# Performance work log

Measured on AMD Instinct MI355X. Metric: run time of the kernel, lower is better.

The kernel has to match this reference:

```python
import jax, jax.numpy as jnp
import numpy as np

T, B, N, D, H = 128, 64, 24, 256, 8
F = D // H  # 32


def setup_inputs() -> dict:
    key = jax.random.key(0)
    ks = jax.random.split(key, 7)
    s = 1.0 / np.sqrt(D)  # torch nn.Linear default init range
    inputs = jax.random.normal(ks[0], (T, B, N * D), dtype=jnp.float32)
    Wk = jax.random.uniform(ks[1], (H, F, D), minval=-s, maxval=s, dtype=jnp.float32)
    bk = jax.random.uniform(ks[2], (H, F), minval=-s, maxval=s, dtype=jnp.float32)
    Wv = jax.random.uniform(ks[3], (H, F, D), minval=-s, maxval=s, dtype=jnp.float32)
    bv = jax.random.uniform(ks[4], (H, F), minval=-s, maxval=s, dtype=jnp.float32)
    Wq = jax.random.uniform(ks[5], (H, N, F, D), minval=-s, maxval=s, dtype=jnp.float32)
    bq = jax.random.uniform(ks[6], (H, N, F), minval=-s, maxval=s, dtype=jnp.float32)
    return {"inputs": inputs, "Wk": Wk, "bk": bk, "Wv": Wv, "bv": bv, "Wq": Wq, "bq": bq}


def reference(inputs, Wk, bk, Wv, bv, Wq, bq):
    # inputs: (T, B, N*D) -> (T, B, N, D)
    x = inputs.reshape(T, B, N, D)
    # shared K/V per head: (T, B, H, N, F)
    k = jnp.einsum('tbnd,hfd->tbhnf', x, Wk) + bk[:, None, :]
    v = jnp.einsum('tbnd,hfd->tbhnf', x, Wv) + bv[:, None, :]
    # per-joint Q: joint n uses its own (F, D) weight -> (T, B, H, N, F)
    q = jnp.einsum('tbnd,hnfd->tbhnf', x, Wq) + bq
    # attention over joints, scaled by sqrt(F)
    scores = jnp.einsum('tbhnf,tbhmf->tbhnm', q, k) / jnp.sqrt(jnp.float32(F))
    attn = jax.nn.softmax(scores, axis=-1)
    out = jnp.einsum('tbhnm,tbhmf->tbhnf', attn, v)
    # concat heads along feature dim per joint, then flatten joints: (T, B, N*H*F)
    out = out.transpose(0, 1, 3, 2, 4).reshape(T, B, N * H * F)
    # dropout is identity in eval mode
    return out
```

## Files before the change

kernel.cpp:

```cpp
#include <hip/hip_runtime.h>
#include <hip/hip_bf16.h>
#include <cstdio>

#define TB  8192
#define N_  24
#define D_  256
#define H_  8
#define F_  32
#define ND  6144
#define HNF 6144

typedef unsigned short u16;
typedef __attribute__((ext_vector_type(8))) _Float16 f16x8;
typedef __attribute__((ext_vector_type(8))) short bf16x8;
typedef __attribute__((ext_vector_type(4))) float f32x4;

__device__ __forceinline__ u16 f2b(float f) {
    unsigned int u = __float_as_uint(f);
    return (u16)((u + 0x7FFFu + ((u >> 16) & 1u)) >> 16);
}
__device__ __forceinline__ float b2f(u16 s) {
    return __uint_as_float(((unsigned int)s) << 16);
}
__device__ __forceinline__ u16 f2h(float f) {
    _Float16 h = (_Float16)f;
    u16 u; __builtin_memcpy(&u, &h, 2); return u;
}

__global__ __launch_bounds__(256) void prep_weights(
    const float* __restrict__ Wk, const float* __restrict__ Wv,
    const float* __restrict__ Wq, u16* __restrict__ Bp)
{
    const int idx = blockIdx.x * 256 + threadIdx.x;
    if (idx >= 24 * 8 * 48 * 64) return;
    const int fr = idx & 15;
    const int fq = (idx >> 4) & 3;
    const int g  = (idx >> 6) % 48;
    const int kt = (idx / (64 * 48)) % 8;
    const int n  = idx / (64 * 48 * 8);
    const int col = g * 16 + fr;
    const int d0  = kt * 32 + fq * 8;
    const int c   = col & 255;
    const float* src;
    if (col < 256)      src = Wk + (size_t)c * 256 + d0;
    else if (col < 512) src = Wv + (size_t)c * 256 + d0;
    else {
        const int h = c >> 5, f = c & 31;
        src = Wq + ((size_t)(h * 24 + n) * 32 + f) * 256 + d0;
    }
    __align__(16) u16 out[8];
    #pragma unroll
    for (int j = 0; j < 8; ++j) out[j] = f2h(src[j]);
    *reinterpret_cast<uint4*>(Bp + (size_t)idx * 8) =
        *reinterpret_cast<const uint4*>(out);
}

__global__ __launch_bounds__(256) void prep_bias(
    const float* __restrict__ bk, const float* __restrict__ bv,
    const float* __restrict__ bq, float* __restrict__ biasp)
{
    const int idx = blockIdx.x * 256 + threadIdx.x;
    if (idx >= 24 * 768) return;
    const int col = idx % 768, n = idx / 768;
    const int c = col & 255;
    float v;
    if (col < 256)      v = bk[c];
    else if (col < 512) v = bv[c];
    else { const int h = c >> 5, f = c & 31; v = bq[(h * 24 + n) * 32 + f]; }
    biasp[n * 768 + col] = v;
}

__global__ __launch_bounds__(512, 2) void proj_mfma(
    const float* __restrict__ x,
    const u16* __restrict__ Bp,
    const float* __restrict__ biasp,
    u16* __restrict__ kb, u16* __restrict__ vb, u16* __restrict__ qb)
{
    const int lin  = blockIdx.x;
    const int n    = (lin & 7) * 3 + ((lin >> 3) >> 7);
    const int mblk = (lin >> 3) & 127;
    const int tb0  = mblk * 64;
    const int tid  = threadIdx.x;
    const int wc   = tid >> 6;
    const int lane = tid & 63;
    const int fr   = lane & 15, fq = lane >> 4;

    __shared__ __align__(16) u16 smem[24576];

    const int arow = tid >> 3;
    const int aq   = tid & 7;
    const int ach  = aq >> 1, ahalf = aq & 1;
    const float* xsrc = x + (size_t)(tb0 + arow) * ND + n * D_ + aq * 4;
    const int awr = (((arow >> 4) * 4 + ach) * 16 + ((arow & 15) ^ ach)) * 8 + ahalf * 4;

    const u16* Bn = Bp + (size_t)n * 8 * 48 * 512;

    f32x4 acc[4][6];
    #pragma unroll
    for (int t = 0; t < 4; ++t)
        #pragma unroll
        for (int j = 0; j < 6; ++j) acc[t][j] = (f32x4){0.f, 0.f, 0.f, 0.f};

    f16x8 bA[6], bB[6];

    {
        const float4 xa = *reinterpret_cast<const float4*>(xsrc);
        const u16* bsrc = Bn + ((size_t)wc * 6) * 512 + lane * 8;
        #pragma unroll
        for (int j = 0; j < 6; ++j)
            bA[j] = *reinterpret_cast<const f16x8*>(bsrc + j * 512);
        ushort4 hv;
        hv.x = f2h(xa.x); hv.y = f2h(xa.y); hv.z = f2h(xa.z); hv.w = f2h(xa.w);
        *reinterpret_cast<ushort4*>(&smem[awr]) = hv;
    }

    #pragma unroll
    for (int kt = 0; kt < 8; ++kt) {
        __syncthreads();
        f16x8 afr[4];
        #pragma unroll
        for (int t = 0; t < 4; ++t)
            afr[t] = *reinterpret_cast<const f16x8*>(
                &smem[(kt & 1) * 2048 + ((t * 4 + fq) * 16 + (fr ^ fq)) * 8]);

        float4 xn;
        if (kt < 7) {
            const u16* bsrc = Bn + ((size_t)(kt + 1) * 48 + wc * 6) * 512 + lane * 8;
            #pragma unroll
            for (int j = 0; j < 6; ++j)
                ((kt & 1) ? bA : bB)[j] = *reinterpret_cast<const f16x8*>(bsrc + j * 512);
            xn = *reinterpret_cast<const float4*>(xsrc + (kt + 1) * 32);
        }

        const f16x8* bc = (kt & 1) ? bB : bA;
        #pragma unroll
        for (int j = 0; j < 6; ++j)
            #pragma unroll
            for (int t = 0; t < 4; ++t)
                acc[t][j] = __builtin_amdgcn_mfma_f32_16x16x32_f16(
                    afr[t], bc[j], acc[t][j], 0, 0, 0);

        if (kt < 7) {
            ushort4 hv;
            hv.x = f2h(xn.x); hv.y = f2h(xn.y); hv.z = f2h(xn.z); hv.w = f2h(xn.w);
            *reinterpret_cast<ushort4*>(&smem[((kt + 1) & 1) * 2048 + awr]) = hv;
        }
    }

    char* outc = (char*)smem;
    #pragma unroll
    for (int p = 0; p < 2; ++p) {
        __syncthreads();
        #pragma unroll
        for (int tt = 0; tt < 2; ++tt) {
            const int t = p * 2 + tt;
            #pragma unroll
            for (int j = 0; j < 6; ++j) {
                const int col = wc * 96 + j * 16 + fr;
                const float bs = biasp[n * 768 + col];
                #pragma unroll
                for (int r = 0; r < 4; ++r) {
                    const int rl = tt * 16 + fq * 4 + r;
                    *reinterpret_cast<u16*>(outc + rl * 1536 +
                        ((col * 2) ^ (((rl >> 2) & 7) << 4))) = f2b(acc[t][j][r] + bs);
                }
            }
        }
        __syncthreads();
        #pragma unroll
        for (int i = 0; i < 6; ++i) {
            const int id  = i * 512 + tid;
            const int rl  = id / 96;
            const int c   = id % 96;
            const uint4 v = *reinterpret_cast<const uint4*>(
                outc + rl * 1536 + ((c * 16) ^ (((rl >> 2) & 7) << 4)));
            const int col0 = c * 8;
            const int kind = col0 >> 8;
            const int cc   = col0 & 255;
            const int h    = cc >> 5, f0 = cc & 31;
            u16* dst = (kind == 0) ? kb : (kind == 1) ? vb : qb;
            const size_t di = (size_t)(tb0 + p * 32 + rl) * HNF + h * (N_ * F_) + n * F_ + f0;
            *reinterpret_cast<uint4*>(&dst[di]) = v;
        }
    }
}

__device__ __forceinline__ int swz(int row, int chunk) {
    return row * 32 + (((chunk ^ ((row >> 1) ^ (row >> 3))) & 3) << 3);
}

__global__ __launch_bounds__(256) void attn_mfma(
    const u16* __restrict__ kb,
    const u16* __restrict__ vb,
    const u16* __restrict__ qb,
    float* __restrict__ out)
{
    const int tid  = threadIdx.x;
    const int wid  = tid >> 6;
    const int lane = tid & 63;
    const int fr   = lane & 15;
    const int fq   = lane >> 4;
    const size_t tb = (size_t)blockIdx.x * 4 + wid;

    __shared__ __align__(16) u16 lds[4][2048];
    u16* Pw = lds[wid];
    u16* Vt = lds[wid] + 1024;

    #pragma unroll
    for (int i = 0; i < 4; ++i)
        reinterpret_cast<uint4*>(lds[wid])[lane + i * 64] = (uint4){0, 0, 0, 0};

    const u16* qt = qb + tb * HNF;
    const u16* kt = kb + tb * HNF;
    const u16* vt = vb + tb * HNF;
    float* outp = out + tb * ND;

    const float scale = 0.17677669529663687f;
    const bool colok = fr < 8;

    for (int h = 0; h < H_; ++h) {
        const u16* qh = qt + h * 768;
        const u16* kh = kt + h * 768;
        const u16* vh = vt + h * 768;

        bf16x8 qa[2], ka[2];
        #pragma unroll
        for (int t = 0; t < 2; ++t) {
            int rq = t * 16 + fr; rq = rq < 24 ? rq : 23;
            qa[t] = *reinterpret_cast<const bf16x8*>(qh + rq * 32 + fq * 8);
            ka[t] = *reinterpret_cast<const bf16x8*>(kh + rq * 32 + fq * 8);
        }

        {
            const int m = lane >> 2, q = lane & 3;
            const uint4 vv = *reinterpret_cast<const uint4*>(vh + m * 32 + q * 8);
            #pragma unroll
            for (int j = 0; j < 8; ++j) {
                const int f = q * 8 + j;
                Vt[swz(f, m >> 3) + (m & 7)] = reinterpret_cast<const u16*>(&vv)[j];
            }
            if (lane < 32) {
                const int m2 = 16 + (lane >> 2), q2 = lane & 3;
                const uint4 v2 = *reinterpret_cast<const uint4*>(vh + m2 * 32 + q2 * 8);
                #pragma unroll
                for (int j = 0; j < 8; ++j) {
                    const int f = q2 * 8 + j;
                    Vt[swz(f, m2 >> 3) + (m2 & 7)] = reinterpret_cast<const u16*>(&v2)[j];
                }
            }
        }

        f32x4 S[2][2];
        #pragma unroll
        for (int a = 0; a < 2; ++a)
            #pragma unroll
            for (int b = 0; b < 2; ++b)
                S[a][b] = __builtin_amdgcn_mfma_f32_16x16x32_bf16(
                    qa[a], ka[b], (f32x4){0.f, 0.f, 0.f, 0.f}, 0, 0, 0);

        float inv[2][4];
        #pragma unroll
        for (int t = 0; t < 2; ++t) {
            const int rowbase = t * 16 + fq * 4;
            float e0[4], e1[4];
            #pragma unroll
            for (int r = 0; r < 4; ++r) {
                const float a = S[t][0][r] * scale;
                const float b = colok ? S[t][1][r] * scale : -1e30f;
                float mx = fmaxf(a, b);
                #pragma unroll
                for (int off = 1; off < 16; off <<= 1)
                    mx = fmaxf(mx, __shfl_xor(mx, off));
                e0[r] = __expf(a - mx);
                e1[r] = colok ? __expf(b - mx) : 0.f;
                float sm = e0[r] + e1[r];
                #pragma unroll
                for (int off = 1; off < 16; off <<= 1)
                    sm += __shfl_xor(sm, off);
                inv[t][r] = 1.f / sm;
            }
            #pragma unroll
            for (int r = 0; r < 4; ++r) {
                const int row = rowbase + r;
                if (row < 24) {
                    Pw[swz(row, fr >> 3) + (fr & 7)] = f2b(e0[r]);
                    if (colok) {
                        const int c1 = 16 + fr;
                        Pw[swz(row, c1 >> 3) + (c1 & 7)] = f2b(e1[r]);
                    }
                }
            }
        }

        bf16x8 pa[2], vbf[2];
        #pragma unroll
        for (int t = 0; t < 2; ++t)
            pa[t] = *reinterpret_cast<const bf16x8*>(&Pw[swz(t * 16 + fr, fq)]);
        #pragma unroll
        for (int t = 0; t < 2; ++t)
            vbf[t] = *reinterpret_cast<const bf16x8*>(&Vt[swz(t * 16 + fr, fq)]);

        f32x4 O[2][2];
        #pragma unroll
        for (int a = 0; a < 2; ++a)
            #pragma unroll
            for (int b = 0; b < 2; ++b)
                O[a][b] = __builtin_amdgcn_mfma_f32_16x16x32_bf16(
                    pa[a], vbf[b], (f32x4){0.f, 0.f, 0.f, 0.f}, 0, 0, 0);

        #pragma unroll
        for (int a = 0; a < 2; ++a)
            #pragma unroll
            for (int r = 0; r < 4; ++r) {
                const int row = a * 16 + fq * 4 + r;
                if (row < 24) {
                    outp[row * D_ + h * F_ + fr]      = O[a][0][r] * inv[a][r];
                    outp[row * D_ + h * F_ + 16 + fr] = O[a][1][r] * inv[a][r];
                }
            }
    }
}

extern "C" void kernel_launch(void* const* d_in, const int* in_sizes, int n_in,
                              void* d_out, int out_size, void* d_ws, size_t ws_size,
                              hipStream_t stream) {
    const float* x  = (const float*)d_in[0];
    const float* Wk = (const float*)d_in[1];
    const float* bk = (const float*)d_in[2];
    const float* Wv = (const float*)d_in[3];
    const float* bv = (const float*)d_in[4];
    const float* Wq = (const float*)d_in[5];
    const float* bq = (const float*)d_in[6];
    float* out = (float*)d_out;

    const size_t qkv_elems = (size_t)TB * HNF;
    const size_t need = qkv_elems * 2ull * 3ull;
    if (ws_size < need) fprintf(stderr, "ws too small: %zu < %zu\n", ws_size, need);
    u16* kbuf = (u16*)d_ws;
    u16* vbuf = kbuf + qkv_elems;
    u16* qbuf = vbuf + qkv_elems;

    u16*   Bp    = (u16*)d_out;
    float* biasp = (float*)((char*)d_out + (size_t)24 * 8 * 48 * 512 * 2);

    prep_weights<<<2304, 256, 0, stream>>>(Wk, Wv, Wq, Bp);
    prep_bias<<<(24 * 768 + 255) / 256, 256, 0, stream>>>(bk, bv, bq, biasp);
    proj_mfma<<<3072, 512, 0, stream>>>(x, Bp, biasp, kbuf, vbuf, qbuf);
    attn_mfma<<<TB / 4, 256, 0, stream>>>(kbuf, vbuf, qbuf, out);
}
```

Baseline: 339.6 us.

## Retile projection GEMM to 128x256 tiles with direct global-to-LDS loads

The projection kernel is restructured so each block computes a 128-row by 256-column tile (one of K, V or Q for one joint) with a 2x4 wave grid. Raw fp32 x and prepacked weights are now copied straight into LDS with global_load_lds, and fp32 is converted to fp16 at fragment read time. This replaces the earlier register-staged double-buffered 64x768 tile. It aims to cut register pressure (launch bounds raised to 4 blocks per CU) and per-thread global load overhead. The cost is that x is re-read for each of the three column tiles and there is no software prefetch across k-steps.

Result: no change. 337.1 us (-0.7%).

```diff
diff --git a/kernel.cpp b/kernel.cpp
--- a/kernel.cpp
+++ b/kernel.cpp
@@ -25,6 +25,12 @@
 __device__ __forceinline__ u16 f2h(float f) {
     _Float16 h = (_Float16)f;
     u16 u; __builtin_memcpy(&u, &h, 2); return u;
+}
+
+__device__ __forceinline__ void gl_lds16(const void* g, void* l) {
+    __builtin_amdgcn_global_load_lds(
+        (const __attribute__((address_space(1))) unsigned int*)g,
+        (__attribute__((address_space(3))) unsigned int*)l, 16, 0, 0);
 }
 
 __global__ __launch_bounds__(256) void prep_weights(
@@ -70,118 +76,105 @@
     biasp[n * 768 + col] = v;
 }
 
-__global__ __launch_bounds__(512, 2) void proj_mfma(
+__global__ __launch_bounds__(512, 4) void proj_mfma(
     const float* __restrict__ x,
     const u16* __restrict__ Bp,
     const float* __restrict__ biasp,
     u16* __restrict__ kb, u16* __restrict__ vb, u16* __restrict__ qb)
 {
     const int lin  = blockIdx.x;
-    const int n    = (lin & 7) * 3 + ((lin >> 3) >> 7);
-    const int mblk = (lin >> 3) & 127;
-    const int tb0  = mblk * 64;
+    const int mblk = lin & 63;
+    const int ct   = (lin >> 6) % 3;
+    const int n    = lin / 192;
+    const int tb0  = mblk * 128;
     const int tid  = threadIdx.x;
-    const int wc   = tid >> 6;
+    const int w    = tid >> 6;
     const int lane = tid & 63;
+    const int wm   = w >> 2;
+    const int wn   = w & 3;
     const int fr   = lane & 15, fq = lane >> 4;
 
-    __shared__ __align__(16) u16 smem[24576];
-
-    const int arow = tid >> 3;
-    const int aq   = tid & 7;
-    const int ach  = aq >> 1, ahalf = aq & 1;
-    const float* xsrc = x + (size_t)(tb0 + arow) * ND + n * D_ + aq * 4;
-    const int awr = (((arow >> 4) * 4 + ach) * 16 + ((arow & 15) ^ ach)) * 8 + ahalf * 4;
-
-    const u16* Bn = Bp + (size_t)n * 8 * 48 * 512;
-
-    f32x4 acc[4][6];
-    #pragma unroll
-    for (int t = 0; t < 4; ++t)
-        #pragma unroll
-        for (int j = 0; j < 6; ++j) acc[t][j] = (f32x4){0.f, 0.f, 0.f, 0.f};
-
-    f16x8 bA[6], bB[6];
-
-    {
-        const float4 xa = *reinterpret_cast<const float4*>(xsrc);
-        const u16* bsrc = Bn + ((size_t)wc * 6) * 512 + lane * 8;
-        #pragma unroll
-        for (int j = 0; j < 6; ++j)
-            bA[j] = *reinterpret_cast<const f16x8*>(bsrc + j * 512);
-        ushort4 hv;
-        hv.x = f2h(xa.x); hv.y = f2h(xa.y); hv.z = f2h(xa.z); hv.w = f2h(xa.w);
-        *reinterpret_cast<ushort4*>(&smem[awr]) = hv;
-    }
-
-    #pragma unroll
+    __shared__ __align__(16) u16 smem[32768];
+    char* Ab = (char*)smem;
+    char* Bb = (char*)smem + 16384;
+
+    const int arow0 = w * 16 + (lane >> 3);
+    const int aclog = (lane & 7) ^ ((lane >> 3) & 7);
+    const char* asrc0 = (const char*)x +
+        (size_t)(tb0 + arow0) * (ND * 4) + n * 1024 + aclog * 16;
+
+    const char* bsrc0 = (const char*)Bp +
+        ((size_t)(n * 8) * 48 + ct * 16 + w * 2) * 1024 + (size_t)lane * 16;
+
+    f32x4 acc[4][4];
+    #pragma unroll
+    for (int m = 0; m < 4; ++m)
+        #pragma unroll
+        for (int j = 0; j < 4; ++j) acc[m][j] = (f32x4){0.f, 0.f, 0.f, 0.f};
+
     for (int kt = 0; kt < 8; ++kt) {
+        #pragma unroll
+        for (int q = 0; q < 2; ++q) {
+            gl_lds16(asrc0 + (size_t)q * (8 * ND * 4) + kt * 128,
+                     Ab + (w * 2 + q) * 1024);
+            gl_lds16(bsrc0 + (size_t)kt * 49152 + q * 1024,
+                     Bb + (w * 2 + q) * 1024);
+        }
         __syncthreads();
-        f16x8 afr[4];
-        #pragma unroll
-        for (int t = 0; t < 4; ++t)
-            afr[t] = *reinterpret_cast<const f16x8*>(
-                &smem[(kt & 1) * 2048 + ((t * 4 + fq) * 16 + (fr ^ fq)) * 8]);
-
-        float4 xn;
-        if (kt < 7) {
-            const u16* bsrc = Bn + ((size_t)(kt + 1) * 48 + wc * 6) * 512 + lane * 8;
-            #pragma unroll
-            for (int j = 0; j < 6; ++j)
-                ((kt & 1) ? bA : bB)[j] = *reinterpret_cast<const f16x8*>(bsrc + j * 512);
-            xn = *reinterpret_cast<const float4*>(xsrc + (kt + 1) * 32);
-        }
-
-        const f16x8* bc = (kt & 1) ? bB : bA;
-        #pragma unroll
-        for (int j = 0; j < 6; ++j)
-            #pragma unroll
-            for (int t = 0; t < 4; ++t)
-                acc[t][j] = __builtin_amdgcn_mfma_f32_16x16x32_f16(
-                    afr[t], bc[j], acc[t][j], 0, 0, 0);
-
-        if (kt < 7) {
-            ushort4 hv;
-            hv.x = f2h(xn.x); hv.y = f2h(xn.y); hv.z = f2h(xn.z); hv.w = f2h(xn.w);
-            *reinterpret_cast<ushort4*>(&smem[((kt + 1) & 1) * 2048 + awr]) = hv;
-        }
-    }
-
-    char* outc = (char*)smem;
-    #pragma unroll
-    for (int p = 0; p < 2; ++p) {
+
+        f16x8 bfr[4];
+        #pragma unroll
+        for (int j = 0; j < 4; ++j)
+            bfr[j] = *reinterpret_cast<const f16x8*>(
+                Bb + ((wn * 4 + j) * 64 + fq * 16 + fr) * 16);
+
+        #pragma unroll
+        for (int m = 0; m < 4; ++m) {
+            const int rowL = wm * 64 + m * 16 + fr;
+            const int c0 = (2 * fq) ^ (fr & 7);
+            const f32x4 lo = *reinterpret_cast<const f32x4*>(Ab + rowL * 128 + c0 * 16);
+            const f32x4 hi = *reinterpret_cast<const f32x4*>(Ab + rowL * 128 + (c0 ^ 1) * 16);
+            f16x8 af;
+            #pragma unroll
+            for (int e = 0; e < 4; ++e) {
+                af[e]     = (_Float16)lo[e];
+                af[4 + e] = (_Float16)hi[e];
+            }
+            #pragma unroll
+            for (int j = 0; j < 4; ++j)
+                acc[m][j] = __builtin_amdgcn_mfma_f32_16x16x32_f16(
+                    af, bfr[j], acc[m][j], 0, 0, 0);
+        }
         __syncthreads();
-        #pragma unroll
-        for (int tt = 0; tt < 2; ++tt) {
-            const int t = p * 2 + tt;
-            #pragma unroll
-            for (int j = 0; j < 6; ++j) {
-                const int col = wc * 96 + j * 16 + fr;
-                const float bs = biasp[n * 768 + col];
-                #pragma unroll
-                for (int r = 0; r < 4; ++r) {
-                    const int rl = tt * 16 + fq * 4 + r;
-                    *reinterpret_cast<u16*>(outc + rl * 1536 +
-                        ((col * 2) ^ (((rl >> 2) & 7) << 4))) = f2b(acc[t][j][r] + bs);
-                }
-            }
-        }
-        __syncthreads();
-        #pragma unroll
-        for (int i = 0; i < 6; ++i) {
-            const int id  = i * 512 + tid;
-            const int rl  = id / 96;
-            const int c   = id % 96;
-            const uint4 v = *reinterpret_cast<const uint4*>(
-                outc + rl * 1536 + ((c * 16) ^ (((rl >> 2) & 7) << 4)));
-            const int col0 = c * 8;
-            const int kind = col0 >> 8;
-            const int cc   = col0 & 255;
-            const int h    = cc >> 5, f0 = cc & 31;
-            u16* dst = (kind == 0) ? kb : (kind == 1) ? vb : qb;
-            const size_t di = (size_t)(tb0 + p * 32 + rl) * HNF + h * (N_ * F_) + n * F_ + f0;
-            *reinterpret_cast<uint4*>(&dst[di]) = v;
-        }
+    }
+
+    #pragma unroll
+    for (int j = 0; j < 4; ++j) {
+        const int colL = wn * 64 + j * 16 + fr;
+        const float bs = biasp[n * 768 + ct * 256 + colL];
+        #pragma unroll
+        for (int m = 0; m < 4; ++m)
+            #pragma unroll
+            for (int r = 0; r < 4; ++r) {
+                const int rowL = wm * 64 + m * 16 + fq * 4 + r;
+                const int byte = (rowL * 512 + colL * 2) ^ ((rowL & 7) << 4);
+                *reinterpret_cast<u16*>((char*)smem + byte) = f2b(acc[m][j][r] + bs);
+            }
+    }
+    __syncthreads();
+
+    u16* dst = (ct == 0) ? kb : (ct == 1) ? vb : qb;
+    #pragma unroll
+    for (int it = 0; it < 8; ++it) {
+        const int id  = it * 512 + tid;
+        const int row = id >> 5;
+        const int c   = id & 31;
+        const uint4 v = *reinterpret_cast<const uint4*>(
+            (char*)smem + (row * 512 + ((c * 16) ^ ((row & 7) << 4))));
+        const int cc = c * 8;
+        const int h  = cc >> 5, f0 = cc & 31;
+        *reinterpret_cast<uint4*>(
+            &dst[(size_t)(tb0 + row) * HNF + h * 768 + n * 32 + f0]) = v;
     }
 }
 
@@ -261,7 +254,6 @@
         float inv[2][4];
         #pragma unroll
         for (int t = 0; t < 2; ++t) {
-            const int rowbase = t * 16 + fq * 4;
             float e0[4], e1[4];
             #pragma unroll
             for (int r = 0; r < 4; ++r) {
@@ -281,7 +273,7 @@
             }
             #pragma unroll
             for (int r = 0; r < 4; ++r) {
-                const int row = rowbase + r;
+                const int row = t * 16 + fq * 4 + r;
                 if (row < 24) {
                     Pw[swz(row, fr >> 3) + (fr & 7)] = f2b(e0[r]);
                     if (colok) {
@@ -345,6 +337,6 @@
 
     prep_weights<<<2304, 256, 0, stream>>>(Wk, Wv, Wq, Bp);
     prep_bias<<<(24 * 768 + 255) / 256, 256, 0, stream>>>(bk, bv, bq, biasp);
-    proj_mfma<<<3072, 512, 0, stream>>>(x, Bp, biasp, kbuf, vbuf, qbuf);
+    proj_mfma<<<4608, 512, 0, stream>>>(x, Bp, biasp, kbuf, vbuf, qbuf);
     attn_mfma<<<TB / 4, 256, 0, stream>>>(kbuf, vbuf, qbuf, out);
 }
```
